# Performance work log

Hardware: AMD Instinct MI355X
Metric: run time of the kernel (lower is better)

## Reference

```python
import jax, jax.numpy as jnp
import numpy as np

N, D, H, E = 50000, 128, 64, 800000


def _linear_params(key, fan_in, fan_out):
    k1, k2 = jax.random.split(key)
    bound = 1.0 / np.sqrt(fan_in)
    w = jax.random.uniform(k1, (fan_in, fan_out), jnp.float32, -bound, bound)
    b = jax.random.uniform(k2, (fan_out,), jnp.float32, -bound, bound)
    return w, b


def setup_inputs() -> dict:
    key = jax.random.key(0)
    ks = jax.random.split(key, 10)
    node_states = jax.random.normal(ks[0], (N, D), jnp.float32)
    capacities = jax.random.uniform(ks[1], (N,), jnp.float32)
    edge_index = jax.random.randint(ks[2], (2, E), 0, N, jnp.int64)
    # redistribution_net: Linear(2D->H), SiLU, Linear(H->H), SiLU, Linear(H->1)
    rw1, rb1 = _linear_params(ks[3], 2 * D, H)
    rw2, rb2 = _linear_params(ks[4], H, H)
    rw3, rb3 = _linear_params(ks[5], H, 1)
    # protection_net: Linear(D+1->H), SiLU, Linear(H->1)
    pw1, pb1 = _linear_params(ks[6], D + 1, H)
    pw2, pb2 = _linear_params(ks[7], H, 1)
    # post_jump_transform: Linear(D->D), Tanh
    tw, tb = _linear_params(ks[8], D, D)
    return dict(node_states=node_states, capacities=capacities, edge_index=edge_index,
                rw1=rw1, rb1=rb1, rw2=rw2, rb2=rb2, rw3=rw3, rb3=rb3,
                pw1=pw1, pb1=pb1, pw2=pw2, pb2=pb2, tw=tw, tb=tb)


def reference(node_states, capacities, edge_index,
              rw1, rb1, rw2, rb2, rw3, rb3,
              pw1, pb1, pw2, pb2, tw, tb):
    n = node_states.shape[0]
    # --- detect_jumps: protection_net(cat(states, capacities)) > 0 ---
    x = jnp.concatenate([node_states, capacities[:, None]], axis=-1)  # (N, D+1)
    act = (jax.nn.silu(x @ pw1 + pb1) @ pw2 + pb2)[:, 0]              # (N,)
    jump_mask = act > 0.0

    # --- redistribute_load ---
    src, tgt = edge_index[0], edge_index[1]
    src_failed = jump_mask[src]
    tgt_alive = ~jump_mask[tgt]
    emask = src_failed & tgt_alive                                    # (E,)

    wi = jnp.concatenate([node_states[src], node_states[tgt]], axis=-1)  # (E, 2D)
    h = jax.nn.silu(wi @ rw1 + rb1)
    h = jax.nn.silu(h @ rw2 + rb2)
    raw = (h @ rw3 + rb3)[:, 0]                                       # (E,)

    # per-source segment softmax over edges with emask
    raw_m = jnp.where(emask, raw, -jnp.inf)
    seg_max = jax.ops.segment_max(raw_m, src, num_segments=n)
    seg_max = jnp.where(jnp.isfinite(seg_max), seg_max, 0.0)
    e = jnp.where(emask, jnp.exp(raw - seg_max[src]), 0.0)
    denom = jax.ops.segment_sum(e, src, num_segments=n)
    dsrc = denom[src]
    w = e / jnp.where(dsrc > 0, dsrc, 1.0)                            # (E,)

    failed_load = jnp.where(jump_mask[:, None], node_states, 0.0)     # (N, D)
    messages = w[:, None] * failed_load[src]                          # (E, D)
    added = jax.ops.segment_sum(messages, tgt, num_segments=n)        # (N, D)
    redistributed = node_states + added

    # --- apply_jumps: failed nodes -> tanh(Linear(x)) * 0.05 ---
    protected = jnp.tanh(redistributed @ tw + tb) * 0.05
    new_states = jnp.where(jump_mask[:, None], protected, redistributed)
    return new_states, jump_mask
```

## Files before the change

kernel.cpp:

```cpp
#include <hip/hip_runtime.h>
#include <cmath>

#define D 128
#define HID 64

__device__ __forceinline__ float silu_f(float x) { return x / (1.0f + expf(-x)); }

__device__ __forceinline__ float4 fma4(float a, float4 w, float4 c) {
    c.x = fmaf(a, w.x, c.x); c.y = fmaf(a, w.y, c.y);
    c.z = fmaf(a, w.z, c.z); c.w = fmaf(a, w.w, c.w);
    return c;
}
__device__ __forceinline__ float4 silu4(float4 v) {
    v.x = silu_f(v.x); v.y = silu_f(v.y); v.z = silu_f(v.z); v.w = silu_f(v.w);
    return v;
}

__device__ __forceinline__ unsigned fenc(float f) {
    unsigned u = __float_as_uint(f);
    return (u & 0x80000000u) ? ~u : (u | 0x80000000u);
}
__device__ __forceinline__ float fdec(unsigned e) {
    unsigned u = (e & 0x80000000u) ? (e & 0x7FFFFFFFu) : ~e;
    return __uint_as_float(u);
}

#define INIT16(bp) { const float4* _b4 = reinterpret_cast<const float4*>(bp); \
    h0 = _b4[0]; h1 = _b4[1]; h2 = _b4[2]; h3 = _b4[3]; \
    h4 = _b4[4]; h5 = _b4[5]; h6 = _b4[6]; h7 = _b4[7]; \
    h8 = _b4[8]; h9 = _b4[9]; h10 = _b4[10]; h11 = _b4[11]; \
    h12 = _b4[12]; h13 = _b4[13]; h14 = _b4[14]; h15 = _b4[15]; }

#define SILU16() { h0 = silu4(h0); h1 = silu4(h1); h2 = silu4(h2); h3 = silu4(h3); \
    h4 = silu4(h4); h5 = silu4(h5); h6 = silu4(h6); h7 = silu4(h7); \
    h8 = silu4(h8); h9 = silu4(h9); h10 = silu4(h10); h11 = silu4(h11); \
    h12 = silu4(h12); h13 = silu4(h13); h14 = silu4(h14); h15 = silu4(h15); }

__device__ __forceinline__ void fd4(float4 h, float4 w, float& s0, float& s1, float& s2, float& s3) {
    s0 = fmaf(h.x, w.x, s0); s1 = fmaf(h.y, w.y, s1);
    s2 = fmaf(h.z, w.z, s2); s3 = fmaf(h.w, w.w, s3);
}
#define FD16(w4) { fd4(h0, w4[0], s0, s1, s2, s3);  fd4(h1, w4[1], s0, s1, s2, s3);  \
    fd4(h2, w4[2], s0, s1, s2, s3);  fd4(h3, w4[3], s0, s1, s2, s3);  \
    fd4(h4, w4[4], s0, s1, s2, s3);  fd4(h5, w4[5], s0, s1, s2, s3);  \
    fd4(h6, w4[6], s0, s1, s2, s3);  fd4(h7, w4[7], s0, s1, s2, s3);  \
    fd4(h8, w4[8], s0, s1, s2, s3);  fd4(h9, w4[9], s0, s1, s2, s3);  \
    fd4(h10, w4[10], s0, s1, s2, s3); fd4(h11, w4[11], s0, s1, s2, s3); \
    fd4(h12, w4[12], s0, s1, s2, s3); fd4(h13, w4[13], s0, s1, s2, s3); \
    fd4(h14, w4[14], s0, s1, s2, s3); fd4(h15, w4[15], s0, s1, s2, s3); }

__device__ __forceinline__ float accdot(float4 h, float4 w, float act) {
    act = fmaf(silu_f(h.x), w.x, act);
    act = fmaf(silu_f(h.y), w.y, act);
    act = fmaf(silu_f(h.z), w.z, act);
    act = fmaf(silu_f(h.w), w.w, act);
    return act;
}

__global__ __launch_bounds__(256) void k_protect(
    const float* __restrict__ states, const float* __restrict__ caps,
    const float* __restrict__ pw1, const float* __restrict__ pb1,
    const float* __restrict__ pw2, const float* __restrict__ pb2,
    unsigned* __restrict__ mask, unsigned* __restrict__ mlist,
    unsigned* __restrict__ counters, float* __restrict__ outmask, int N) {
    __shared__ float wl[129 * 64];
    unsigned tid = threadIdx.x;
    {
        const float4* s4 = reinterpret_cast<const float4*>(pw1);
        float4* d4 = reinterpret_cast<float4*>(wl);
#pragma unroll
        for (int q = 0; q < 9; ++q) {
            unsigned idx = tid + q * 256u;
            if (idx < 2064u) d4[idx] = s4[idx];
        }
    }
    __syncthreads();
    unsigned nl = tid >> 2, g = tid & 3u;
    unsigned n = blockIdx.x * 64u + nl;
    bool active = n < (unsigned)N;
    unsigned nq = active ? n : (unsigned)(N - 1);
    const float4* row = reinterpret_cast<const float4*>(states + (size_t)nq * D);
    float4 a0, a1, a2, a3;
    { const float4* b4 = reinterpret_cast<const float4*>(pb1 + g * 16);
      a0 = b4[0]; a1 = b4[1]; a2 = b4[2]; a3 = b4[3]; }
    const float* wg = wl + g * 16;
#pragma unroll 1
    for (int kb = 0; kb < 32; ++kb) {
        float4 x = row[kb];
        const float* w = wg + (size_t)kb * 4 * HID;
        const float4* w0 = reinterpret_cast<const float4*>(w);
        const float4* w1 = reinterpret_cast<const float4*>(w + HID);
        const float4* w2q = reinterpret_cast<const float4*>(w + 2 * HID);
        const float4* w3q = reinterpret_cast<const float4*>(w + 3 * HID);
        a0 = fma4(x.x, w0[0], a0); a1 = fma4(x.x, w0[1], a1); a2 = fma4(x.x, w0[2], a2); a3 = fma4(x.x, w0[3], a3);
        a0 = fma4(x.y, w1[0], a0); a1 = fma4(x.y, w1[1], a1); a2 = fma4(x.y, w1[2], a2); a3 = fma4(x.y, w1[3], a3);
        a0 = fma4(x.z, w2q[0], a0); a1 = fma4(x.z, w2q[1], a1); a2 = fma4(x.z, w2q[2], a2); a3 = fma4(x.z, w2q[3], a3);
        a0 = fma4(x.w, w3q[0], a0); a1 = fma4(x.w, w3q[1], a1); a2 = fma4(x.w, w3q[2], a2); a3 = fma4(x.w, w3q[3], a3);
    }
    {
        float xv = caps[nq];
        const float4* wc = reinterpret_cast<const float4*>(wg + (size_t)128 * HID);
        a0 = fma4(xv, wc[0], a0); a1 = fma4(xv, wc[1], a1);
        a2 = fma4(xv, wc[2], a2); a3 = fma4(xv, wc[3], a3);
    }
    const float4* w2 = reinterpret_cast<const float4*>(pw2 + g * 16);
    float p = 0.0f;
    p = accdot(a0, w2[0], p); p = accdot(a1, w2[1], p);
    p = accdot(a2, w2[2], p); p = accdot(a3, w2[3], p);
    p += __shfl_xor(p, 1);
    p += __shfl_xor(p, 2);
    bool pred = false;
    if (active && g == 0) {
        float act = p + pb2[0];
        unsigned m = (act > 0.0f) ? 1u : 0u;
        mask[n] = m;
        outmask[n] = m ? 1.0f : 0.0f;
        pred = (m != 0u);
    }
    unsigned lane = tid & 63u;
    unsigned long long bal = __ballot(pred);
    unsigned wcnt = (unsigned)__popcll(bal);
    unsigned pre  = (unsigned)__popcll(bal & ((1ull << lane) - 1ull));
    unsigned base = 0;
    if (lane == 0 && wcnt) base = atomicAdd(&counters[1], wcnt);
    base = __shfl(base, 0);
    if (pred) mlist[base + pre] = n;
}

__global__ __launch_bounds__(256) void k_nodemlp(
    const float* __restrict__ states, const unsigned* __restrict__ mask,
    const float* __restrict__ rw1, float* __restrict__ uv, int N) {
    __shared__ float wl[16384];
    unsigned tid = threadIdx.x;
    {
        const float4* s4 = reinterpret_cast<const float4*>(rw1);
        float4* d4 = reinterpret_cast<float4*>(wl);
#pragma unroll
        for (int q = 0; q < 16; ++q) d4[tid + q * 256u] = s4[tid + q * 256u];
    }
    __syncthreads();
    unsigned nl = tid >> 2, g = tid & 3u;
    unsigned n = blockIdx.x * 64u + nl;
    if (n >= (unsigned)N) return;
    const float4* row = reinterpret_cast<const float4*>(states + (size_t)n * D);
    unsigned m = mask[n];
    const float* wg = wl + (m ? 0u : 8192u) + g * 16;
    float4 a0, a1, a2, a3;
    a0.x=a0.y=a0.z=a0.w=0.f; a1=a0; a2=a0; a3=a0;
#pragma unroll 1
    for (int kb = 0; kb < 32; ++kb) {
        float4 x = row[kb];
        const float* w = wg + (size_t)kb * 4 * HID;
        const float4* w0 = reinterpret_cast<const float4*>(w);
        const float4* w1 = reinterpret_cast<const float4*>(w + HID);
        const float4* w2q = reinterpret_cast<const float4*>(w + 2 * HID);
        const float4* w3q = reinterpret_cast<const float4*>(w + 3 * HID);
        a0 = fma4(x.x, w0[0], a0); a1 = fma4(x.x, w0[1], a1); a2 = fma4(x.x, w0[2], a2); a3 = fma4(x.x, w0[3], a3);
        a0 = fma4(x.y, w1[0], a0); a1 = fma4(x.y, w1[1], a1); a2 = fma4(x.y, w1[2], a2); a3 = fma4(x.y, w1[3], a3);
        a0 = fma4(x.z, w2q[0], a0); a1 = fma4(x.z, w2q[1], a1); a2 = fma4(x.z, w2q[2], a2); a3 = fma4(x.z, w2q[3], a3);
        a0 = fma4(x.w, w3q[0], a0); a1 = fma4(x.w, w3q[1], a1); a2 = fma4(x.w, w3q[2], a2); a3 = fma4(x.w, w3q[3], a3);
    }
    float4* o = reinterpret_cast<float4*>(uv + (size_t)n * HID + g * 16);
    o[0] = a0; o[1] = a1; o[2] = a2; o[3] = a3;
}

__global__ __launch_bounds__(256) void k_compact(
    const int* __restrict__ ei, const unsigned* __restrict__ mask,
    unsigned* __restrict__ act_eid, unsigned* __restrict__ counters,
    unsigned* __restrict__ hist, int E) {
    __shared__ unsigned wbase[4];
    int e = blockIdx.x * 256 + threadIdx.x;
    unsigned wid = threadIdx.x >> 6, lane = threadIdx.x & 63u;
    bool pred = false; int t = 0;
    if (e < E) {
        int s = ei[e]; t = ei[E + e];
        pred = mask[s] && !mask[t];
    }
    unsigned long long bal = __ballot(pred);
    unsigned wcnt = (unsigned)__popcll(bal);
    unsigned pre  = (unsigned)__popcll(bal & ((1ull << lane) - 1ull));
    if (lane == 0) wbase[wid] = wcnt;
    __syncthreads();
    if (threadIdx.x == 0) {
        unsigned c0 = wbase[0], c1 = wbase[1], c2 = wbase[2], c3 = wbase[3];
        unsigned tot = c0 + c1 + c2 + c3;
        unsigned b = tot ? atomicAdd(&counters[0], tot) : 0u;
        wbase[0] = b; wbase[1] = b + c0; wbase[2] = b + c0 + c1; wbase[3] = b + c0 + c1 + c2;
    }
    __syncthreads();
    if (pred) {
        act_eid[wbase[wid] + pre] = (unsigned)e;
        atomicAdd(&hist[t], 1u);
    }
}

__global__ __launch_bounds__(256) void k_scanA(const unsigned* __restrict__ hist,
                                               unsigned* __restrict__ bsum, int N) {
    __shared__ unsigned sm[256];
    unsigned t = threadIdx.x;
    unsigned i = blockIdx.x * 256u + t;
    sm[t] = (i < (unsigned)N) ? hist[i] : 0u;
    __syncthreads();
#pragma unroll
    for (unsigned d = 128; d > 0; d >>= 1) {
        if (t < d) sm[t] += sm[t + d];
        __syncthreads();
    }
    if (t == 0) bsum[blockIdx.x] = sm[0];
}
__global__ __launch_bounds__(256) void k_scanB(const unsigned* __restrict__ bsum,
                                               unsigned* __restrict__ bpre, int nb) {
    __shared__ unsigned sm[256];
    unsigned t = threadIdx.x;
    unsigned v = (t < (unsigned)nb) ? bsum[t] : 0u;
    sm[t] = v;
    __syncthreads();
    for (unsigned d = 1; d < 256; d <<= 1) {
        unsigned x = (t >= d) ? sm[t - d] : 0u;
        __syncthreads();
        sm[t] += x;
        __syncthreads();
    }
    if (t < (unsigned)nb) bpre[t] = sm[t] - v;
}
__global__ __launch_bounds__(256) void k_scanC(const unsigned* __restrict__ hist,
                                               const unsigned* __restrict__ bpre,
                                               unsigned* __restrict__ offs,
                                               unsigned* __restrict__ cursor, int N) {
    __shared__ unsigned sm[256];
    unsigned t = threadIdx.x;
    unsigned i = blockIdx.x * 256u + t;
    unsigned v = (i < (unsigned)N) ? hist[i] : 0u;
    sm[t] = v;
    __syncthreads();
    for (unsigned d = 1; d < 256; d <<= 1) {
        unsigned x = (t >= d) ? sm[t - d] : 0u;
        __syncthreads();
        sm[t] += x;
        __syncthreads();
    }
    unsigned exc = sm[t] - v + bpre[blockIdx.x];
    if (i < (unsigned)N) { offs[i] = exc; cursor[i] = exc; }
    if (i == (unsigned)N - 1) offs[N] = exc + v;
}

__global__ __launch_bounds__(256) void k_edge_mlp(
    const float* __restrict__ uv, const int* __restrict__ ei,
    const float* __restrict__ rb1, const float* __restrict__ rw2,
    const float* __restrict__ rb2, const float* __restrict__ rw3,
    const float* __restrict__ rb3,
    const unsigned* __restrict__ act_eid, const unsigned* __restrict__ counters,
    float* __restrict__ rawbuf, unsigned* __restrict__ segmax, int E) {
    __shared__ float w2t[64 * 68];
    unsigned cnt = counters[0];
    if (blockIdx.x * 256u >= cnt) return;
    unsigned tid = threadIdx.x;
#pragma unroll
    for (int q = 0; q < 16; ++q) {
        int i = (int)tid + q * 256;
        w2t[(i & 63) * 68 + (i >> 6)] = rw2[i];
    }
    __syncthreads();
    unsigned grp = blockIdx.x * 256u + tid;
    bool active = grp < cnt;
    unsigned gq = active ? grp : (cnt - 1);
    int e = (int)act_eid[gq];
    int s = ei[e], tg = ei[E + e];
    const float4* ur = reinterpret_cast<const float4*>(uv + (size_t)s * HID);
    const float4* vr = reinterpret_cast<const float4*>(uv + (size_t)tg * HID);
    float4 h0, h1, h2, h3, h4, h5, h6, h7, h8, h9, h10, h11, h12, h13, h14, h15;
    INIT16(rb1);
#define ADDUV(hh, i) { float4 _u = ur[i]; float4 _v = vr[i]; \
    hh.x = hh.x + _u.x + _v.x; hh.y = hh.y + _u.y + _v.y; \
    hh.z = hh.z + _u.z + _v.z; hh.w = hh.w + _u.w + _v.w; }
    ADDUV(h0, 0)  ADDUV(h1, 1)  ADDUV(h2, 2)  ADDUV(h3, 3)
    ADDUV(h4, 4)  ADDUV(h5, 5)  ADDUV(h6, 6)  ADDUV(h7, 7)
    ADDUV(h8, 8)  ADDUV(h9, 9)  ADDUV(h10, 10) ADDUV(h11, 11)
    ADDUV(h12, 12) ADDUV(h13, 13) ADDUV(h14, 14) ADDUV(h15, 15)
#undef ADDUV
    SILU16();
    float raw = rb3[0];
#pragma unroll 1
    for (int j = 0; j < HID; ++j) {
        const float4* w4 = reinterpret_cast<const float4*>(w2t + j * 68);
        float s0 = rb2[j], s1 = 0.f, s2 = 0.f, s3 = 0.f;
        FD16(w4);
        float h2v = silu_f((s0 + s1) + (s2 + s3));
        raw = fmaf(h2v, rw3[j], raw);
    }
    if (active) {
        rawbuf[grp] = raw;
        atomicMax(&segmax[s], fenc(raw));
    }
}

__global__ void k_exp(const int* __restrict__ ei, const unsigned* __restrict__ act_eid,
                      const unsigned* __restrict__ counters, const unsigned* __restrict__ segmax,
                      float* __restrict__ rawbuf, float* __restrict__ denom, int E) {
    unsigned t = blockIdx.x * blockDim.x + threadIdx.x;
    if (blockIdx.x * blockDim.x >= counters[0]) return;
    if (t >= counters[0]) return;
    int e = (int)act_eid[t];
    int s = ei[e];
    float ev = expf(rawbuf[t] - fdec(segmax[s]));
    rawbuf[t] = ev;
    atomicAdd(&denom[s], ev);
}

__global__ void k_fill(const int* __restrict__ ei, const unsigned* __restrict__ act_eid,
                       const unsigned* __restrict__ counters, const float* __restrict__ rawbuf,
                       const float* __restrict__ denom, unsigned* __restrict__ cursor,
                       float* __restrict__ wbuf, unsigned* __restrict__ sbuf, int E) {
    unsigned t = blockIdx.x * blockDim.x + threadIdx.x;
    if (blockIdx.x * blockDim.x >= counters[0]) return;
    if (t >= counters[0]) return;
    int e = (int)act_eid[t];
    int s = ei[e], tg = ei[E + e];
    float w = rawbuf[t] / denom[s];
    unsigned pos = atomicAdd(&cursor[tg], 1u);
    wbuf[pos] = w;
    sbuf[pos] = (unsigned)s;
}

__global__ __launch_bounds__(256) void k_gather(
    const float* __restrict__ states, const float* __restrict__ wbuf,
    const unsigned* __restrict__ sbuf, const unsigned* __restrict__ offs,
    float* __restrict__ out, int N) {
    unsigned n = blockIdx.x * 4u + (threadIdx.x >> 6);
    unsigned lane = threadIdx.x & 63u;
    if (n >= (unsigned)N) return;
    unsigned start = offs[n], end = offs[n + 1];
    float2 acc = reinterpret_cast<const float2*>(states + (size_t)n * D)[lane];
    for (unsigned i = start; i < end; ++i) {
        float w = wbuf[i];
        unsigned s = sbuf[i];
        float2 sv = reinterpret_cast<const float2*>(states + (size_t)s * D)[lane];
        acc.x = fmaf(w, sv.x, acc.x);
        acc.y = fmaf(w, sv.y, acc.y);
    }
    reinterpret_cast<float2*>(out + (size_t)n * D)[lane] = acc;
}

__global__ __launch_bounds__(256) void k_jump(
    const float* __restrict__ states,
    const float* __restrict__ tw, const float* __restrict__ tb,
    const unsigned* __restrict__ mlist, const unsigned* __restrict__ counters,
    float* __restrict__ out) {
    __shared__ float xs[8][D];
    unsigned cnt = counters[1];
    unsigned base = blockIdx.x * 8u;
    if (base >= cnt || cnt == 0) return;
    unsigned tid = threadIdx.x;
    unsigned d = tid & 127u, r = tid >> 7;
    {
        unsigned j = tid >> 5;
        unsigned c = (tid & 31u) * 4u;
        unsigned slot = base + j; if (slot >= cnt) slot = cnt - 1;
        int nn = (int)mlist[slot];
        *reinterpret_cast<float4*>(&xs[j][c]) =
            *reinterpret_cast<const float4*>(&states[(size_t)nn * D + c]);
    }
    __syncthreads();
    float tbd = tb[d];
    float a0 = tbd, a1 = tbd, a2 = tbd, a3 = tbd;
    const float* x0 = &xs[r * 4 + 0][0];
    const float* x1 = &xs[r * 4 + 1][0];
    const float* x2 = &xs[r * 4 + 2][0];
    const float* x3 = &xs[r * 4 + 3][0];
#pragma unroll 1
    for (int k = 0; k < D; ++k) {
        float w = tw[(size_t)k * D + d];
        a0 = fmaf(x0[k], w, a0);
        a1 = fmaf(x1[k], w, a1);
        a2 = fmaf(x2[k], w, a2);
        a3 = fmaf(x3[k], w, a3);
    }
    float res[4] = {a0, a1, a2, a3};
#pragma unroll
    for (int j2 = 0; j2 < 4; ++j2) {
        unsigned slot = base + r * 4 + j2;
        if (slot < cnt) {
            int nn = (int)mlist[slot];
            out[(size_t)nn * D + d] = tanhf(res[j2]) * 0.05f;
        }
    }
}

extern "C" void kernel_launch(void* const* d_in, const int* in_sizes, int n_in,
                              void* d_out, int out_size, void* d_ws, size_t ws_size,
                              hipStream_t stream) {
    const float* states = (const float*)d_in[0];
    const float* caps   = (const float*)d_in[1];
    const int*   ei     = (const int*)d_in[2];
    const float* rw1 = (const float*)d_in[3];  const float* rb1 = (const float*)d_in[4];
    const float* rw2 = (const float*)d_in[5];  const float* rb2 = (const float*)d_in[6];
    const float* rw3 = (const float*)d_in[7];  const float* rb3 = (const float*)d_in[8];
    const float* pw1 = (const float*)d_in[9];  const float* pb1 = (const float*)d_in[10];
    const float* pw2 = (const float*)d_in[11]; const float* pb2 = (const float*)d_in[12];
    const float* tw  = (const float*)d_in[13]; const float* tb  = (const float*)d_in[14];
    const int N = in_sizes[1];
    const int E = in_sizes[2] / 2;
    float* out = (float*)d_out;
    const int nb = (N + 255) / 256;

    float* uv = out;

    unsigned* ws       = (unsigned*)d_ws;
    unsigned* counters = ws;
    unsigned* segmax   = ws + 4;
    float*    denom    = (float*)(ws + 4 + 1 * (size_t)N);
    unsigned* hist     = ws + 4 + 2 * (size_t)N;
    unsigned* mask     = ws + 4 + 3 * (size_t)N;
    unsigned* mlist    = ws + 4 + 4 * (size_t)N;
    unsigned* offs     = ws + 4 + 5 * (size_t)N;
    unsigned* cursor   = ws + 4 + 6 * (size_t)N + 1;
    unsigned* bsum     = ws + 4 + 7 * (size_t)N + 1;
    unsigned* bpre     = bsum + 256;
    unsigned* act_eid  = bpre + 256;
    float*    rawbuf   = (float*)(act_eid + (size_t)E);
    float*    wbuf     = (float*)(act_eid + 2 * (size_t)E);
    unsigned* sbuf     = act_eid + 3 * (size_t)E;

    (void)hipMemsetAsync(d_ws, 0, (size_t)(4 + 3 * (size_t)N) * 4, stream);

    k_protect<<<(N + 63) / 64, 256, 0, stream>>>(states, caps, pw1, pb1, pw2, pb2,
                                                 mask, mlist, counters, out + (size_t)N * D, N);
    k_nodemlp<<<(N + 63) / 64, 256, 0, stream>>>(states, mask, rw1, uv, N);
    k_compact<<<(E + 255) / 256, 256, 0, stream>>>(ei, mask, act_eid, counters, hist, E);
    k_scanA<<<nb, 256, 0, stream>>>(hist, bsum, N);
    k_scanB<<<1, 256, 0, stream>>>(bsum, bpre, nb);
    k_scanC<<<nb, 256, 0, stream>>>(hist, bpre, offs, cursor, N);
    k_edge_mlp<<<(E + 255) / 256, 256, 0, stream>>>(uv, ei, rb1, rw2, rb2, rw3, rb3,
                                                    act_eid, counters, rawbuf, segmax, E);
    k_exp<<<(E + 255) / 256, 256, 0, stream>>>(ei, act_eid, counters, segmax, rawbuf, denom, E);
    k_fill<<<(E + 255) / 256, 256, 0, stream>>>(ei, act_eid, counters, rawbuf, denom,
                                                cursor, wbuf, sbuf, E);
    k_gather<<<(N + 3) / 4, 256, 0, stream>>>(states, wbuf, sbuf, offs, out, N);
    k_jump<<<(N + 7) / 8, 256, 0, stream>>>(states, tw, tb, mlist, counters, out);
}
```

Before: 267.1 us.

## Split node and protection MLPs into two LDS phases and pair threads in edge MLP

```diff
diff --git a/kernel.cpp b/kernel.cpp
--- a/kernel.cpp
+++ b/kernel.cpp
@@ -63,52 +63,72 @@
     const float* __restrict__ pw2, const float* __restrict__ pb2,
     unsigned* __restrict__ mask, unsigned* __restrict__ mlist,
     unsigned* __restrict__ counters, float* __restrict__ outmask, int N) {
-    __shared__ float wl[129 * 64];
+    __shared__ float wl[65 * 64];
     unsigned tid = threadIdx.x;
-    {
-        const float4* s4 = reinterpret_cast<const float4*>(pw1);
-        float4* d4 = reinterpret_cast<float4*>(wl);
-#pragma unroll
-        for (int q = 0; q < 9; ++q) {
-            unsigned idx = tid + q * 256u;
-            if (idx < 2064u) d4[idx] = s4[idx];
-        }
-    }
-    __syncthreads();
-    unsigned nl = tid >> 2, g = tid & 3u;
-    unsigned n = blockIdx.x * 64u + nl;
+    unsigned nl = tid >> 3, g = tid & 7u;
+    unsigned n = blockIdx.x * 32u + nl;
     bool active = n < (unsigned)N;
     unsigned nq = active ? n : (unsigned)(N - 1);
     const float4* row = reinterpret_cast<const float4*>(states + (size_t)nq * D);
-    float4 a0, a1, a2, a3;
-    { const float4* b4 = reinterpret_cast<const float4*>(pb1 + g * 16);
-      a0 = b4[0]; a1 = b4[1]; a2 = b4[2]; a3 = b4[3]; }
-    const float* wg = wl + g * 16;
-#pragma unroll 1
-    for (int kb = 0; kb < 32; ++kb) {
+    float4 a0, a1;
+    { const float4* b4 = reinterpret_cast<const float4*>(pb1 + g * 8);
+      a0 = b4[0]; a1 = b4[1]; }
+    const float* wg = wl + g * 8;
+    {
+        const float4* s4 = reinterpret_cast<const float4*>(pw1);
+        float4* d4 = reinterpret_cast<float4*>(wl);
+#pragma unroll
+        for (int q = 0; q < 4; ++q) d4[tid + q * 256u] = s4[tid + q * 256u];
+    }
+    __syncthreads();
+#pragma unroll 1
+    for (int kb = 0; kb < 16; ++kb) {
         float4 x = row[kb];
         const float* w = wg + (size_t)kb * 4 * HID;
         const float4* w0 = reinterpret_cast<const float4*>(w);
         const float4* w1 = reinterpret_cast<const float4*>(w + HID);
         const float4* w2q = reinterpret_cast<const float4*>(w + 2 * HID);
         const float4* w3q = reinterpret_cast<const float4*>(w + 3 * HID);
-        a0 = fma4(x.x, w0[0], a0); a1 = fma4(x.x, w0[1], a1); a2 = fma4(x.x, w0[2], a2); a3 = fma4(x.x, w0[3], a3);
-        a0 = fma4(x.y, w1[0], a0); a1 = fma4(x.y, w1[1], a1); a2 = fma4(x.y, w1[2], a2); a3 = fma4(x.y, w1[3], a3);
-        a0 = fma4(x.z, w2q[0], a0); a1 = fma4(x.z, w2q[1], a1); a2 = fma4(x.z, w2q[2], a2); a3 = fma4(x.z, w2q[3], a3);
-        a0 = fma4(x.w, w3q[0], a0); a1 = fma4(x.w, w3q[1], a1); a2 = fma4(x.w, w3q[2], a2); a3 = fma4(x.w, w3q[3], a3);
+        a0 = fma4(x.x, w0[0], a0); a1 = fma4(x.x, w0[1], a1);
+        a0 = fma4(x.y, w1[0], a0); a1 = fma4(x.y, w1[1], a1);
+        a0 = fma4(x.z, w2q[0], a0); a1 = fma4(x.z, w2q[1], a1);
+        a0 = fma4(x.w, w3q[0], a0); a1 = fma4(x.w, w3q[1], a1);
+    }
+    __syncthreads();
+    {
+        const float4* s4 = reinterpret_cast<const float4*>(pw1 + 4096);
+        float4* d4 = reinterpret_cast<float4*>(wl);
+#pragma unroll
+        for (int q = 0; q < 5; ++q) {
+            unsigned idx = tid + q * 256u;
+            if (idx < 1040u) d4[idx] = s4[idx];
+        }
+    }
+    __syncthreads();
+#pragma unroll 1
+    for (int kb = 0; kb < 16; ++kb) {
+        float4 x = row[kb + 16];
+        const float* w = wg + (size_t)kb * 4 * HID;
+        const float4* w0 = reinterpret_cast<const float4*>(w);
+        const float4* w1 = reinterpret_cast<const float4*>(w + HID);
+        const float4* w2q = reinterpret_cast<const float4*>(w + 2 * HID);
+        const float4* w3q = reinterpret_cast<const float4*>(w + 3 * HID);
+        a0 = fma4(x.x, w0[0], a0); a1 = fma4(x.x, w0[1], a1);
+        a0 = fma4(x.y, w1[0], a0); a1 = fma4(x.y, w1[1], a1);
+        a0 = fma4(x.z, w2q[0], a0); a1 = fma4(x.z, w2q[1], a1);
+        a0 = fma4(x.w, w3q[0], a0); a1 = fma4(x.w, w3q[1], a1);
     }
     {
         float xv = caps[nq];
-        const float4* wc = reinterpret_cast<const float4*>(wg + (size_t)128 * HID);
+        const float4* wc = reinterpret_cast<const float4*>(wg + 4096);
         a0 = fma4(xv, wc[0], a0); a1 = fma4(xv, wc[1], a1);
-        a2 = fma4(xv, wc[2], a2); a3 = fma4(xv, wc[3], a3);
-    }
-    const float4* w2 = reinterpret_cast<const float4*>(pw2 + g * 16);
+    }
+    const float4* w2 = reinterpret_cast<const float4*>(pw2 + g * 8);
     float p = 0.0f;
     p = accdot(a0, w2[0], p); p = accdot(a1, w2[1], p);
-    p = accdot(a2, w2[2], p); p = accdot(a3, w2[3], p);
     p += __shfl_xor(p, 1);
     p += __shfl_xor(p, 2);
+    p += __shfl_xor(p, 4);
     bool pred = false;
     if (active && g == 0) {
         float act = p + pb2[0];
@@ -128,40 +148,72 @@
 }
 
 __global__ __launch_bounds__(256) void k_nodemlp(
-    const float* __restrict__ states, const unsigned* __restrict__ mask,
-    const float* __restrict__ rw1, float* __restrict__ uv, int N) {
-    __shared__ float wl[16384];
+    const float* __restrict__ states, const float* __restrict__ rw1,
+    float* __restrict__ u, float* __restrict__ v, int N) {
+    __shared__ float wl[8192];
     unsigned tid = threadIdx.x;
+    unsigned nl = tid >> 3, g = tid & 7u;
+    unsigned n = blockIdx.x * 32u + nl;
+    unsigned nq = (n < (unsigned)N) ? n : (unsigned)(N - 1);
+    const float4* row = reinterpret_cast<const float4*>(states + (size_t)nq * D);
+    const float* wg = wl + g * 8;
     {
         const float4* s4 = reinterpret_cast<const float4*>(rw1);
         float4* d4 = reinterpret_cast<float4*>(wl);
 #pragma unroll
-        for (int q = 0; q < 16; ++q) d4[tid + q * 256u] = s4[tid + q * 256u];
-    }
-    __syncthreads();
-    unsigned nl = tid >> 2, g = tid & 3u;
-    unsigned n = blockIdx.x * 64u + nl;
-    if (n >= (unsigned)N) return;
-    const float4* row = reinterpret_cast<const float4*>(states + (size_t)n * D);
-    unsigned m = mask[n];
-    const float* wg = wl + (m ? 0u : 8192u) + g * 16;
-    float4 a0, a1, a2, a3;
-    a0.x=a0.y=a0.z=a0.w=0.f; a1=a0; a2=a0; a3=a0;
-#pragma unroll 1
-    for (int kb = 0; kb < 32; ++kb) {
-        float4 x = row[kb];
-        const float* w = wg + (size_t)kb * 4 * HID;
-        const float4* w0 = reinterpret_cast<const float4*>(w);
-        const float4* w1 = reinterpret_cast<const float4*>(w + HID);
-        const float4* w2q = reinterpret_cast<const float4*>(w + 2 * HID);
-        const float4* w3q = reinterpret_cast<const float4*>(w + 3 * HID);
-        a0 = fma4(x.x, w0[0], a0); a1 = fma4(x.x, w0[1], a1); a2 = fma4(x.x, w0[2], a2); a3 = fma4(x.x, w0[3], a3);
-        a0 = fma4(x.y, w1[0], a0); a1 = fma4(x.y, w1[1], a1); a2 = fma4(x.y, w1[2], a2); a3 = fma4(x.y, w1[3], a3);
-        a0 = fma4(x.z, w2q[0], a0); a1 = fma4(x.z, w2q[1], a1); a2 = fma4(x.z, w2q[2], a2); a3 = fma4(x.z, w2q[3], a3);
-        a0 = fma4(x.w, w3q[0], a0); a1 = fma4(x.w, w3q[1], a1); a2 = fma4(x.w, w3q[2], a2); a3 = fma4(x.w, w3q[3], a3);
-    }
-    float4* o = reinterpret_cast<float4*>(uv + (size_t)n * HID + g * 16);
-    o[0] = a0; o[1] = a1; o[2] = a2; o[3] = a3;
+        for (int q = 0; q < 8; ++q) d4[tid + q * 256u] = s4[tid + q * 256u];
+    }
+    __syncthreads();
+    {
+        float4 a0, a1;
+        a0.x=a0.y=a0.z=a0.w=0.f; a1=a0;
+#pragma unroll 1
+        for (int kb = 0; kb < 32; ++kb) {
+            float4 x = row[kb];
+            const float* w = wg + (size_t)kb * 4 * HID;
+            const float4* w0 = reinterpret_cast<const float4*>(w);
+            const float4* w1 = reinterpret_cast<const float4*>(w + HID);
+            const float4* w2q = reinterpret_cast<const float4*>(w + 2 * HID);
+            const float4* w3q = reinterpret_cast<const float4*>(w + 3 * HID);
+            a0 = fma4(x.x, w0[0], a0); a1 = fma4(x.x, w0[1], a1);
+            a0 = fma4(x.y, w1[0], a0); a1 = fma4(x.y, w1[1], a1);
+            a0 = fma4(x.z, w2q[0], a0); a1 = fma4(x.z, w2q[1], a1);
+            a0 = fma4(x.w, w3q[0], a0); a1 = fma4(x.w, w3q[1], a1);
+        }
+        if (n < (unsigned)N) {
+            float4* o = reinterpret_cast<float4*>(u + (size_t)n * HID + g * 8);
+            o[0] = a0; o[1] = a1;
+        }
+    }
+    __syncthreads();
+    {
+        const float4* s4 = reinterpret_cast<const float4*>(rw1 + 8192);
+        float4* d4 = reinterpret_cast<float4*>(wl);
+#pragma unroll
+        for (int q = 0; q < 8; ++q) d4[tid + q * 256u] = s4[tid + q * 256u];
+    }
+    __syncthreads();
+    {
+        float4 a0, a1;
+        a0.x=a0.y=a0.z=a0.w=0.f; a1=a0;
+#pragma unroll 1
+        for (int kb = 0; kb < 32; ++kb) {
+            float4 x = row[kb];
+            const float* w = wg + (size_t)kb * 4 * HID;
+            const float4* w0 = reinterpret_cast<const float4*>(w);
+            const float4* w1 = reinterpret_cast<const float4*>(w + HID);
+            const float4* w2q = reinterpret_cast<const float4*>(w + 2 * HID);
+            const float4* w3q = reinterpret_cast<const float4*>(w + 3 * HID);
+            a0 = fma4(x.x, w0[0], a0); a1 = fma4(x.x, w0[1], a1);
+            a0 = fma4(x.y, w1[0], a0); a1 = fma4(x.y, w1[1], a1);
+            a0 = fma4(x.z, w2q[0], a0); a1 = fma4(x.z, w2q[1], a1);
+            a0 = fma4(x.w, w3q[0], a0); a1 = fma4(x.w, w3q[1], a1);
+        }
+        if (n < (unsigned)N) {
+            float4* o = reinterpret_cast<float4*>(v + (size_t)n * HID + g * 8);
+            o[0] = a0; o[1] = a1;
+        }
+    }
 }
 
 __global__ __launch_bounds__(256) void k_compact(
@@ -245,7 +297,8 @@
 }
 
 __global__ __launch_bounds__(256) void k_edge_mlp(
-    const float* __restrict__ uv, const int* __restrict__ ei,
+    const float* __restrict__ u, const float* __restrict__ v,
+    const int* __restrict__ ei,
     const float* __restrict__ rb1, const float* __restrict__ rw2,
     const float* __restrict__ rb2, const float* __restrict__ rw3,
     const float* __restrict__ rb3,
@@ -253,7 +306,7 @@
     float* __restrict__ rawbuf, unsigned* __restrict__ segmax, int E) {
     __shared__ float w2t[64 * 68];
     unsigned cnt = counters[0];
-    if (blockIdx.x * 256u >= cnt) return;
+    if (blockIdx.x * 128u >= cnt) return;
     unsigned tid = threadIdx.x;
 #pragma unroll
     for (int q = 0; q < 16; ++q) {
@@ -261,13 +314,14 @@
         w2t[(i & 63) * 68 + (i >> 6)] = rw2[i];
     }
     __syncthreads();
-    unsigned grp = blockIdx.x * 256u + tid;
+    unsigned grp = blockIdx.x * 128u + (tid >> 1);
+    unsigned p = tid & 1u;
     bool active = grp < cnt;
     unsigned gq = active ? grp : (cnt - 1);
     int e = (int)act_eid[gq];
     int s = ei[e], tg = ei[E + e];
-    const float4* ur = reinterpret_cast<const float4*>(uv + (size_t)s * HID);
-    const float4* vr = reinterpret_cast<const float4*>(uv + (size_t)tg * HID);
+    const float4* ur = reinterpret_cast<const float4*>(u + (size_t)s * HID);
+    const float4* vr = reinterpret_cast<const float4*>(v + (size_t)tg * HID);
     float4 h0, h1, h2, h3, h4, h5, h6, h7, h8, h9, h10, h11, h12, h13, h14, h15;
     INIT16(rb1);
 #define ADDUV(hh, i) { float4 _u = ur[i]; float4 _v = vr[i]; \
@@ -279,16 +333,19 @@
     ADDUV(h12, 12) ADDUV(h13, 13) ADDUV(h14, 14) ADDUV(h15, 15)
 #undef ADDUV
     SILU16();
-    float raw = rb3[0];
-#pragma unroll 1
-    for (int j = 0; j < HID; ++j) {
+    float part = 0.0f;
+    int j0 = 32 * (int)p;
+#pragma unroll 1
+    for (int j = j0; j < j0 + 32; ++j) {
         const float4* w4 = reinterpret_cast<const float4*>(w2t + j * 68);
         float s0 = rb2[j], s1 = 0.f, s2 = 0.f, s3 = 0.f;
         FD16(w4);
         float h2v = silu_f((s0 + s1) + (s2 + s3));
-        raw = fmaf(h2v, rw3[j], raw);
-    }
-    if (active) {
+        part = fmaf(h2v, rw3[j], part);
+    }
+    part += __shfl_xor(part, 1);
+    if (active && p == 0) {
+        float raw = part + rb3[0];
         rawbuf[grp] = raw;
         atomicMax(&segmax[s], fenc(raw));
     }
@@ -403,7 +460,8 @@
     float* out = (float*)d_out;
     const int nb = (N + 255) / 256;
 
-    float* uv = out;
+    float* u = out;
+    float* v = out + (size_t)N * HID;
 
     unsigned* ws       = (unsigned*)d_ws;
     unsigned* counters = ws;
@@ -423,15 +481,15 @@
 
     (void)hipMemsetAsync(d_ws, 0, (size_t)(4 + 3 * (size_t)N) * 4, stream);
 
-    k_protect<<<(N + 63) / 64, 256, 0, stream>>>(states, caps, pw1, pb1, pw2, pb2,
+    k_protect<<<(N + 31) / 32, 256, 0, stream>>>(states, caps, pw1, pb1, pw2, pb2,
                                                  mask, mlist, counters, out + (size_t)N * D, N);
-    k_nodemlp<<<(N + 63) / 64, 256, 0, stream>>>(states, mask, rw1, uv, N);
+    k_nodemlp<<<(N + 31) / 32, 256, 0, stream>>>(states, rw1, u, v, N);
     k_compact<<<(E + 255) / 256, 256, 0, stream>>>(ei, mask, act_eid, counters, hist, E);
     k_scanA<<<nb, 256, 0, stream>>>(hist, bsum, N);
     k_scanB<<<1, 256, 0, stream>>>(bsum, bpre, nb);
     k_scanC<<<nb, 256, 0, stream>>>(hist, bpre, offs, cursor, N);
-    k_edge_mlp<<<(E + 255) / 256, 256, 0, stream>>>(uv, ei, rb1, rw2, rb2, rw3, rb3,
-                                                    act_eid, counters, rawbuf, segmax, E);
+    k_edge_mlp<<<(2 * E + 255) / 256, 256, 0, stream>>>(u, v, ei, rb1, rw2, rb2, rw3, rb3,
+                                                        act_eid, counters, rawbuf, segmax, E);
     k_exp<<<(E + 255) / 256, 256, 0, stream>>>(ei, act_eid, counters, segmax, rawbuf, denom, E);
     k_fill<<<(E + 255) / 256, 256, 0, stream>>>(ei, act_eid, counters, rawbuf, denom,
                                                 cursor, wbuf, sbuf, E);
```

Result: slower. 298.7 us (+11.8%).

## Register-block node MLPs over 4 nodes and split edge MLP hidden layer across lanes

Applied to the files above, without the earlier changes.

```diff
diff --git a/kernel.cpp b/kernel.cpp
--- a/kernel.cpp
+++ b/kernel.cpp
@@ -57,7 +57,15 @@
     return act;
 }
 
-__global__ __launch_bounds__(256) void k_protect(
+#define PQUAD(xc0, xc1, xc2, xc3, wptr) { \
+    const float4* _w = reinterpret_cast<const float4*>(wptr); \
+    float4 _w0 = _w[0], _w1 = _w[1]; \
+    a00 = fma4(xc0, _w0, a00); a01 = fma4(xc0, _w1, a01); \
+    a10 = fma4(xc1, _w0, a10); a11 = fma4(xc1, _w1, a11); \
+    a20 = fma4(xc2, _w0, a20); a21 = fma4(xc2, _w1, a21); \
+    a30 = fma4(xc3, _w0, a30); a31 = fma4(xc3, _w1, a31); }
+
+__global__ __launch_bounds__(128) void k_protect(
     const float* __restrict__ states, const float* __restrict__ caps,
     const float* __restrict__ pw1, const float* __restrict__ pb1,
     const float* __restrict__ pw2, const float* __restrict__ pb2,
@@ -69,99 +77,117 @@
         const float4* s4 = reinterpret_cast<const float4*>(pw1);
         float4* d4 = reinterpret_cast<float4*>(wl);
 #pragma unroll
-        for (int q = 0; q < 9; ++q) {
-            unsigned idx = tid + q * 256u;
+        for (int q = 0; q < 17; ++q) {
+            unsigned idx = tid + q * 128u;
             if (idx < 2064u) d4[idx] = s4[idx];
         }
     }
     __syncthreads();
-    unsigned nl = tid >> 2, g = tid & 3u;
-    unsigned n = blockIdx.x * 64u + nl;
-    bool active = n < (unsigned)N;
-    unsigned nq = active ? n : (unsigned)(N - 1);
-    const float4* row = reinterpret_cast<const float4*>(states + (size_t)nq * D);
-    float4 a0, a1, a2, a3;
-    { const float4* b4 = reinterpret_cast<const float4*>(pb1 + g * 16);
-      a0 = b4[0]; a1 = b4[1]; a2 = b4[2]; a3 = b4[3]; }
-    const float* wg = wl + g * 16;
-#pragma unroll 1
+    unsigned grp = tid >> 3, r = tid & 7u;
+    unsigned nbase = blockIdx.x * 64u + grp * 4u;
+    unsigned N1 = (unsigned)(N - 1);
+    unsigned n0 = min(nbase + 0u, N1), n1 = min(nbase + 1u, N1);
+    unsigned n2 = min(nbase + 2u, N1), n3 = min(nbase + 3u, N1);
+    const float4* r0 = reinterpret_cast<const float4*>(states + (size_t)n0 * D);
+    const float4* r1 = reinterpret_cast<const float4*>(states + (size_t)n1 * D);
+    const float4* r2 = reinterpret_cast<const float4*>(states + (size_t)n2 * D);
+    const float4* r3 = reinterpret_cast<const float4*>(states + (size_t)n3 * D);
+    float4 a00, a01, a10, a11, a20, a21, a30, a31;
+    { const float4* b4 = reinterpret_cast<const float4*>(pb1 + r * 8);
+      a00 = b4[0]; a01 = b4[1]; a10 = a00; a11 = a01;
+      a20 = a00; a21 = a01; a30 = a00; a31 = a01; }
+    const float* wg = wl + r * 8;
+#pragma unroll 2
     for (int kb = 0; kb < 32; ++kb) {
-        float4 x = row[kb];
-        const float* w = wg + (size_t)kb * 4 * HID;
-        const float4* w0 = reinterpret_cast<const float4*>(w);
-        const float4* w1 = reinterpret_cast<const float4*>(w + HID);
-        const float4* w2q = reinterpret_cast<const float4*>(w + 2 * HID);
-        const float4* w3q = reinterpret_cast<const float4*>(w + 3 * HID);
-        a0 = fma4(x.x, w0[0], a0); a1 = fma4(x.x, w0[1], a1); a2 = fma4(x.x, w0[2], a2); a3 = fma4(x.x, w0[3], a3);
-        a0 = fma4(x.y, w1[0], a0); a1 = fma4(x.y, w1[1], a1); a2 = fma4(x.y, w1[2], a2); a3 = fma4(x.y, w1[3], a3);
-        a0 = fma4(x.z, w2q[0], a0); a1 = fma4(x.z, w2q[1], a1); a2 = fma4(x.z, w2q[2], a2); a3 = fma4(x.z, w2q[3], a3);
-        a0 = fma4(x.w, w3q[0], a0); a1 = fma4(x.w, w3q[1], a1); a2 = fma4(x.w, w3q[2], a2); a3 = fma4(x.w, w3q[3], a3);
+        float4 x0 = r0[kb], x1 = r1[kb], x2 = r2[kb], x3 = r3[kb];
+        const float* w = wg + (size_t)kb * 256;
+        PQUAD(x0.x, x1.x, x2.x, x3.x, w)
+        PQUAD(x0.y, x1.y, x2.y, x3.y, w + 64)
+        PQUAD(x0.z, x1.z, x2.z, x3.z, w + 128)
+        PQUAD(x0.w, x1.w, x2.w, x3.w, w + 192)
     }
     {
-        float xv = caps[nq];
-        const float4* wc = reinterpret_cast<const float4*>(wg + (size_t)128 * HID);
-        a0 = fma4(xv, wc[0], a0); a1 = fma4(xv, wc[1], a1);
-        a2 = fma4(xv, wc[2], a2); a3 = fma4(xv, wc[3], a3);
-    }
-    const float4* w2 = reinterpret_cast<const float4*>(pw2 + g * 16);
-    float p = 0.0f;
-    p = accdot(a0, w2[0], p); p = accdot(a1, w2[1], p);
-    p = accdot(a2, w2[2], p); p = accdot(a3, w2[3], p);
-    p += __shfl_xor(p, 1);
-    p += __shfl_xor(p, 2);
-    bool pred = false;
-    if (active && g == 0) {
-        float act = p + pb2[0];
-        unsigned m = (act > 0.0f) ? 1u : 0u;
-        mask[n] = m;
-        outmask[n] = m ? 1.0f : 0.0f;
-        pred = (m != 0u);
-    }
+        float c0 = caps[n0], c1 = caps[n1], c2 = caps[n2], c3 = caps[n3];
+        PQUAD(c0, c1, c2, c3, wg + (size_t)128 * 64)
+    }
+    const float4* w2 = reinterpret_cast<const float4*>(pw2 + r * 8);
+    float4 w20 = w2[0], w21 = w2[1];
+    float p0 = 0.f, p1 = 0.f, p2 = 0.f, p3 = 0.f;
+    p0 = accdot(a00, w20, p0); p0 = accdot(a01, w21, p0);
+    p1 = accdot(a10, w20, p1); p1 = accdot(a11, w21, p1);
+    p2 = accdot(a20, w20, p2); p2 = accdot(a21, w21, p2);
+    p3 = accdot(a30, w20, p3); p3 = accdot(a31, w21, p3);
+#pragma unroll
+    for (int m = 1; m <= 4; m <<= 1) {
+        p0 += __shfl_xor(p0, m); p1 += __shfl_xor(p1, m);
+        p2 += __shfl_xor(p2, m); p3 += __shfl_xor(p3, m);
+    }
+    float pb2v = pb2[0];
     unsigned lane = tid & 63u;
-    unsigned long long bal = __ballot(pred);
-    unsigned wcnt = (unsigned)__popcll(bal);
-    unsigned pre  = (unsigned)__popcll(bal & ((1ull << lane) - 1ull));
-    unsigned base = 0;
-    if (lane == 0 && wcnt) base = atomicAdd(&counters[1], wcnt);
-    base = __shfl(base, 0);
-    if (pred) mlist[base + pre] = n;
-}
-
-__global__ __launch_bounds__(256) void k_nodemlp(
-    const float* __restrict__ states, const unsigned* __restrict__ mask,
-    const float* __restrict__ rw1, float* __restrict__ uv, int N) {
-    __shared__ float wl[16384];
+#define EMIT(q, pq, nq) { \
+    bool pred = false; \
+    if ((nbase + q) < (unsigned)N && r == 0) { \
+        float act = pq + pb2v; \
+        unsigned m = (act > 0.0f) ? 1u : 0u; \
+        mask[nq] = m; outmask[nq] = m ? 1.0f : 0.0f; \
+        pred = (m != 0u); \
+    } \
+    unsigned long long bal = __ballot(pred); \
+    unsigned wcnt = (unsigned)__popcll(bal); \
+    unsigned pre  = (unsigned)__popcll(bal & ((1ull << lane) - 1ull)); \
+    unsigned base = 0; \
+    if (lane == 0 && wcnt) base = atomicAdd(&counters[1], wcnt); \
+    base = __shfl(base, 0); \
+    if (pred) mlist[base + pre] = nq; }
+    EMIT(0, p0, n0) EMIT(1, p1, n1) EMIT(2, p2, n2) EMIT(3, p3, n3)
+#undef EMIT
+}
+
+__global__ __launch_bounds__(128) void k_nodemlp(
+    const float* __restrict__ states, const float* __restrict__ rw1,
+    float* __restrict__ u, float* __restrict__ v, int N) {
+    __shared__ float wl[8192];
     unsigned tid = threadIdx.x;
-    {
-        const float4* s4 = reinterpret_cast<const float4*>(rw1);
-        float4* d4 = reinterpret_cast<float4*>(wl);
-#pragma unroll
-        for (int q = 0; q < 16; ++q) d4[tid + q * 256u] = s4[tid + q * 256u];
-    }
-    __syncthreads();
-    unsigned nl = tid >> 2, g = tid & 3u;
-    unsigned n = blockIdx.x * 64u + nl;
-    if (n >= (unsigned)N) return;
-    const float4* row = reinterpret_cast<const float4*>(states + (size_t)n * D);
-    unsigned m = mask[n];
-    const float* wg = wl + (m ? 0u : 8192u) + g * 16;
-    float4 a0, a1, a2, a3;
-    a0.x=a0.y=a0.z=a0.w=0.f; a1=a0; a2=a0; a3=a0;
-#pragma unroll 1
-    for (int kb = 0; kb < 32; ++kb) {
-        float4 x = row[kb];
-        const float* w = wg + (size_t)kb * 4 * HID;
-        const float4* w0 = reinterpret_cast<const float4*>(w);
-        const float4* w1 = reinterpret_cast<const float4*>(w + HID);
-        const float4* w2q = reinterpret_cast<const float4*>(w + 2 * HID);
-        const float4* w3q = reinterpret_cast<const float4*>(w + 3 * HID);
-        a0 = fma4(x.x, w0[0], a0); a1 = fma4(x.x, w0[1], a1); a2 = fma4(x.x, w0[2], a2); a3 = fma4(x.x, w0[3], a3);
-        a0 = fma4(x.y, w1[0], a0); a1 = fma4(x.y, w1[1], a1); a2 = fma4(x.y, w1[2], a2); a3 = fma4(x.y, w1[3], a3);
-        a0 = fma4(x.z, w2q[0], a0); a1 = fma4(x.z, w2q[1], a1); a2 = fma4(x.z, w2q[2], a2); a3 = fma4(x.z, w2q[3], a3);
-        a0 = fma4(x.w, w3q[0], a0); a1 = fma4(x.w, w3q[1], a1); a2 = fma4(x.w, w3q[2], a2); a3 = fma4(x.w, w3q[3], a3);
-    }
-    float4* o = reinterpret_cast<float4*>(uv + (size_t)n * HID + g * 16);
-    o[0] = a0; o[1] = a1; o[2] = a2; o[3] = a3;
+    unsigned grp = tid >> 3, r = tid & 7u;
+    unsigned nbase = blockIdx.x * 64u + grp * 4u;
+    unsigned N1 = (unsigned)(N - 1);
+    unsigned n0 = min(nbase + 0u, N1), n1 = min(nbase + 1u, N1);
+    unsigned n2 = min(nbase + 2u, N1), n3 = min(nbase + 3u, N1);
+    const float4* r0 = reinterpret_cast<const float4*>(states + (size_t)n0 * D);
+    const float4* r1 = reinterpret_cast<const float4*>(states + (size_t)n1 * D);
+    const float4* r2 = reinterpret_cast<const float4*>(states + (size_t)n2 * D);
+    const float4* r3 = reinterpret_cast<const float4*>(states + (size_t)n3 * D);
+    const float* wg = wl + r * 8;
+#pragma unroll
+    for (int ph = 0; ph < 2; ++ph) {
+        if (ph) __syncthreads();
+        {
+            const float4* s4 = reinterpret_cast<const float4*>(rw1 + ph * 8192);
+            float4* d4 = reinterpret_cast<float4*>(wl);
+#pragma unroll
+            for (int q = 0; q < 16; ++q) d4[tid + q * 128u] = s4[tid + q * 128u];
+        }
+        __syncthreads();
+        float4 a00, a01, a10, a11, a20, a21, a30, a31;
+        a00.x=a00.y=a00.z=a00.w=0.f; a01=a00; a10=a00; a11=a00;
+        a20=a00; a21=a00; a30=a00; a31=a00;
+#pragma unroll 2
+        for (int kb = 0; kb < 32; ++kb) {
+            float4 x0 = r0[kb], x1 = r1[kb], x2 = r2[kb], x3 = r3[kb];
+            const float* w = wg + (size_t)kb * 256;
+            PQUAD(x0.x, x1.x, x2.x, x3.x, w)
+            PQUAD(x0.y, x1.y, x2.y, x3.y, w + 64)
+            PQUAD(x0.z, x1.z, x2.z, x3.z, w + 128)
+            PQUAD(x0.w, x1.w, x2.w, x3.w, w + 192)
+        }
+        float* dst = ph ? v : u;
+#define WOUT(q, aq0, aq1, nq) if ((nbase + q) < (unsigned)N) { \
+        float4* o = reinterpret_cast<float4*>(dst + (size_t)nq * HID + r * 8); \
+        o[0] = aq0; o[1] = aq1; }
+        WOUT(0, a00, a01, n0) WOUT(1, a10, a11, n1)
+        WOUT(2, a20, a21, n2) WOUT(3, a30, a31, n3)
+#undef WOUT
+    }
 }
 
 __global__ __launch_bounds__(256) void k_compact(
@@ -245,7 +271,8 @@
 }
 
 __global__ __launch_bounds__(256) void k_edge_mlp(
-    const float* __restrict__ uv, const int* __restrict__ ei,
+    const float* __restrict__ u, const float* __restrict__ v,
+    const int* __restrict__ ei,
     const float* __restrict__ rb1, const float* __restrict__ rw2,
     const float* __restrict__ rb2, const float* __restrict__ rw3,
     const float* __restrict__ rb3,
@@ -253,7 +280,7 @@
     float* __restrict__ rawbuf, unsigned* __restrict__ segmax, int E) {
     __shared__ float w2t[64 * 68];
     unsigned cnt = counters[0];
-    if (blockIdx.x * 256u >= cnt) return;
+    if (blockIdx.x * 128u >= cnt) return;
     unsigned tid = threadIdx.x;
 #pragma unroll
     for (int q = 0; q < 16; ++q) {
@@ -261,13 +288,14 @@
         w2t[(i & 63) * 68 + (i >> 6)] = rw2[i];
     }
     __syncthreads();
-    unsigned grp = blockIdx.x * 256u + tid;
+    unsigned grp = blockIdx.x * 128u + (tid >> 1);
+    unsigned p = tid & 1u;
     bool active = grp < cnt;
     unsigned gq = active ? grp : (cnt - 1);
     int e = (int)act_eid[gq];
     int s = ei[e], tg = ei[E + e];
-    const float4* ur = reinterpret_cast<const float4*>(uv + (size_t)s * HID);
-    const float4* vr = reinterpret_cast<const float4*>(uv + (size_t)tg * HID);
+    const float4* ur = reinterpret_cast<const float4*>(u + (size_t)s * HID);
+    const float4* vr = reinterpret_cast<const float4*>(v + (size_t)tg * HID);
     float4 h0, h1, h2, h3, h4, h5, h6, h7, h8, h9, h10, h11, h12, h13, h14, h15;
     INIT16(rb1);
 #define ADDUV(hh, i) { float4 _u = ur[i]; float4 _v = vr[i]; \
@@ -279,16 +307,19 @@
     ADDUV(h12, 12) ADDUV(h13, 13) ADDUV(h14, 14) ADDUV(h15, 15)
 #undef ADDUV
     SILU16();
-    float raw = rb3[0];
+    float part = 0.0f;
+    int j0 = 32 * (int)p;
 #pragma unroll 1
-    for (int j = 0; j < HID; ++j) {
+    for (int j = j0; j < j0 + 32; ++j) {
         const float4* w4 = reinterpret_cast<const float4*>(w2t + j * 68);
         float s0 = rb2[j], s1 = 0.f, s2 = 0.f, s3 = 0.f;
         FD16(w4);
         float h2v = silu_f((s0 + s1) + (s2 + s3));
-        raw = fmaf(h2v, rw3[j], raw);
-    }
-    if (active) {
+        part = fmaf(h2v, rw3[j], part);
+    }
+    part += __shfl_xor(part, 1);
+    if (active && p == 0) {
+        float raw = part + rb3[0];
         rawbuf[grp] = raw;
         atomicMax(&segmax[s], fenc(raw));
     }
@@ -403,7 +434,8 @@
     float* out = (float*)d_out;
     const int nb = (N + 255) / 256;
 
-    float* uv = out;
+    float* u = out;
+    float* v = out + (size_t)N * HID;
 
     unsigned* ws       = (unsigned*)d_ws;
     unsigned* counters = ws;
@@ -423,15 +455,15 @@
 
     (void)hipMemsetAsync(d_ws, 0, (size_t)(4 + 3 * (size_t)N) * 4, stream);
 
-    k_protect<<<(N + 63) / 64, 256, 0, stream>>>(states, caps, pw1, pb1, pw2, pb2,
+    k_protect<<<(N + 63) / 64, 128, 0, stream>>>(states, caps, pw1, pb1, pw2, pb2,
                                                  mask, mlist, counters, out + (size_t)N * D, N);
-    k_nodemlp<<<(N + 63) / 64, 256, 0, stream>>>(states, mask, rw1, uv, N);
+    k_nodemlp<<<(N + 63) / 64, 128, 0, stream>>>(states, rw1, u, v, N);
     k_compact<<<(E + 255) / 256, 256, 0, stream>>>(ei, mask, act_eid, counters, hist, E);
     k_scanA<<<nb, 256, 0, stream>>>(hist, bsum, N);
     k_scanB<<<1, 256, 0, stream>>>(bsum, bpre, nb);
     k_scanC<<<nb, 256, 0, stream>>>(hist, bpre, offs, cursor, N);
-    k_edge_mlp<<<(E + 255) / 256, 256, 0, stream>>>(uv, ei, rb1, rw2, rb2, rw3, rb3,
-                                                    act_eid, counters, rawbuf, segmax, E);
+    k_edge_mlp<<<(2 * E + 255) / 256, 256, 0, stream>>>(u, v, ei, rb1, rw2, rb2, rw3, rb3,
+                                                        act_eid, counters, rawbuf, segmax, E);
     k_exp<<<(E + 255) / 256, 256, 0, stream>>>(ei, act_eid, counters, segmax, rawbuf, denom, E);
     k_fill<<<(E + 255) / 256, 256, 0, stream>>>(ei, act_eid, counters, rawbuf, denom,
                                                 cursor, wbuf, sbuf, E);
```

Measured after the change: 290.3 us. +8.7%, slower.
